# Kernel optimization log

Hardware: AMD Instinct MI355X
Metric: run time of the kernel (lower is better)

The kernel has to match this reference:

```python
import jax, jax.numpy as jnp
import numpy as np

B, H, T, K, V = 4, 16, 2048, 128, 128


def setup_inputs() -> dict:
    key = jax.random.key(0)
    ks = jax.random.split(key, 5)
    q = jax.random.normal(ks[0], (B, H, T, K), dtype=jnp.float32)
    k = jax.random.normal(ks[1], (B, H, T, K), dtype=jnp.float32)
    v = jax.random.normal(ks[2], (B, H, T, V), dtype=jnp.float32)
    # g is a per-step log decay gate: small negative so exp(g) in (0.95, 1]
    g = -jax.random.uniform(ks[3], (B, H, T), dtype=jnp.float32) * 0.05
    # beta is the delta-rule step size, in (0, 1)
    beta = jax.random.uniform(ks[4], (B, H, T), dtype=jnp.float32)
    initial_state = jnp.zeros((B, H, K, V), dtype=jnp.float32)
    return {"q": q, "k": k, "v": v, "g": g, "beta": beta,
            "initial_state": initial_state}


def _l2norm(x, eps=1e-12):
    # matches F.normalize(p=2, dim=-1): x / max(||x||_2, eps)
    n = jnp.sqrt(jnp.sum(x * x, axis=-1, keepdims=True))
    return x / jnp.maximum(n, eps)


def reference(q, k, v, g, beta, initial_state):
    q = _l2norm(q)
    k = _l2norm(k)
    scale = q.shape[-1] ** -0.5  # default scale of chunk_gated_delta_rule

    # time-major for scan: [T, B, H, ...]
    qT = jnp.moveaxis(q, 2, 0) * scale
    kT = jnp.moveaxis(k, 2, 0)
    vT = jnp.moveaxis(v, 2, 0)
    gT = jnp.moveaxis(g, 2, 0)
    bT = jnp.moveaxis(beta, 2, 0)

    def step(S, inp):
        qt, kt, vt, gt, bt = inp  # qt/kt: [B,H,K], vt: [B,H,V], gt/bt: [B,H]
        S = S * jnp.exp(gt)[..., None, None]           # gated decay of state
        kS = jnp.einsum('bhk,bhkv->bhv', kt, S)        # current prediction
        dv = bt[..., None] * (vt - kS)                 # delta-rule correction
        S = S + jnp.einsum('bhk,bhv->bhkv', kt, dv)    # rank-1 state update
        ot = jnp.einsum('bhk,bhkv->bhv', qt, S)        # readout
        return S, ot

    final_state, oT = jax.lax.scan(step, initial_state, (qT, kT, vT, gT, bT))
    o = jnp.moveaxis(oT, 0, 2)  # [B,H,T,V]
    return o, final_state
```

## Files before the change

### kernel.cpp

```cpp
#include <hip/hip_runtime.h>
#include <math.h>

typedef float f32x16 __attribute__((ext_vector_type(16)));
typedef short s16x8 __attribute__((ext_vector_type(8)));
typedef unsigned int u32;

namespace {
constexpr int B_ = 4, H_ = 16, T_ = 2048, K_ = 128, V_ = 128;
constexpr int BHn = B_ * H_;
constexpr int C = 32;
constexpr int NCH = T_ / C;
constexpr int NS = 4;
constexpr int VS = V_ / NS;
constexpr float SCALE = 0.08838834764831845f;
constexpr int SK = 136;
constexpr int SRT = 36;
constexpr int SF = 36;
constexpr size_t WSCH = 4608;
}

__device__ __forceinline__ ushort f2bf(float x) {
  unsigned u = __builtin_bit_cast(unsigned, x);
  u += 0x7FFF + ((u >> 16) & 1);
  return (ushort)(u >> 16);
}
__device__ __forceinline__ u32 cvtpk(float lo, float hi) {
  u32 r;
  asm("v_cvt_pk_bf16_f32 %0, %1, %2" : "=v"(r) : "v"(lo), "v"(hi));
  return r;
}
__device__ __forceinline__ int rowmap(int i, int lh) { return (i & 3) + 8 * (i >> 2) + 4 * lh; }

__device__ __forceinline__ void bar_lds() {
  asm volatile("s_waitcnt lgkmcnt(0)" ::: "memory");
  __builtin_amdgcn_s_barrier();
  asm volatile("" ::: "memory");
}

__device__ __forceinline__ s16x8 ld8u(const ushort* p) {
  uint2 a = *(const uint2*)(p);
  uint2 b = *(const uint2*)(p + 4);
  int4 r = make_int4((int)a.x, (int)a.y, (int)b.x, (int)b.y);
  return __builtin_bit_cast(s16x8, r);
}

__device__ __forceinline__ void packq(const f32x16& a, u32* u) {
  #pragma unroll
  for (int j = 0; j < 4; ++j) {
    u[2*j]   = cvtpk(a[4*j],   a[4*j+1]);
    u[2*j+1] = cvtpk(a[4*j+2], a[4*j+3]);
  }
}
__device__ __forceinline__ void swapfr(const u32* u, s16x8& f0, s16x8& f1) {
  u32 a0 = u[0], b0 = u[2], a1 = u[1], b1 = u[3];
  u32 a2 = u[4], b2 = u[6], a3 = u[5], b3 = u[7];
  asm("v_permlane32_swap_b32 %0, %1" : "+v"(a0), "+v"(b0));
  asm("v_permlane32_swap_b32 %0, %1" : "+v"(a1), "+v"(b1));
  asm("v_permlane32_swap_b32 %0, %1" : "+v"(a2), "+v"(b2));
  asm("v_permlane32_swap_b32 %0, %1" : "+v"(a3), "+v"(b3));
  f0 = __builtin_bit_cast(s16x8, make_int4((int)a0, (int)a1, (int)b0, (int)b1));
  f1 = __builtin_bit_cast(s16x8, make_int4((int)a2, (int)a3, (int)b2, (int)b3));
}

#define MFMA __builtin_amdgcn_mfma_f32_32x32x16_bf16

__device__ __forceinline__ f32x16 mm8(const ushort* A, const ushort* B, int lr, int lh) {
  f32x16 a0, a1;
  #pragma unroll
  for (int i = 0; i < 16; ++i) { a0[i] = 0.f; a1[i] = 0.f; }
  #pragma unroll
  for (int kb = 0; kb < 8; kb += 2) {
    const int o0 = lr * SK + 16 * kb + 8 * lh, o1 = o0 + 16;
    a0 = MFMA(*(const s16x8*)(A + o0), *(const s16x8*)(B + o0), a0, 0, 0, 0);
    a1 = MFMA(*(const s16x8*)(A + o1), *(const s16x8*)(B + o1), a1, 0, 0, 0);
  }
  return a0 + a1;
}

__global__ __launch_bounds__(256, 2)
void gdn_pre_kernel(const float* __restrict__ qg, const float* __restrict__ kg,
                    const float* __restrict__ gg, const float* __restrict__ bg,
                    char* __restrict__ ws)
{
  const int bid = blockIdx.x;
  const int bh = bid >> 6, ch = bid & 63;
  const int t = threadIdx.x, w = t >> 6, l = t & 63, lr = l & 31, lh = l >> 5;
  const int r8 = t >> 3, c8 = t & 7;
  const int t0 = ch * C;

  __shared__ __align__(16) ushort Kh[C * SK], Qh[C * SK];
  __shared__ __align__(16) float Mm[C * SF];
  __shared__ __align__(16) ushort Tt[C * 32], Gt[C * 32];
  __shared__ float ls_g[C], ls_b[C], ls_eb[C], ls_emb[C], ls_nq[C];

  {
    const float4* q4 = (const float4*)(qg + ((size_t)bh * T_ + t0 + r8) * K_);
    const float4* k4 = (const float4*)(kg + ((size_t)bh * T_ + t0 + r8) * K_);
    float4 qv[4], kv[4]; float sq = 0.f, sk = 0.f;
    #pragma unroll
    for (int c = 0; c < 4; ++c) {
      qv[c] = q4[c8 + 8 * c]; kv[c] = k4[c8 + 8 * c];
      sq += qv[c].x*qv[c].x + qv[c].y*qv[c].y + qv[c].z*qv[c].z + qv[c].w*qv[c].w;
      sk += kv[c].x*kv[c].x + kv[c].y*kv[c].y + kv[c].z*kv[c].z + kv[c].w*kv[c].w;
    }
    sq += __shfl_xor(sq, 1); sq += __shfl_xor(sq, 2); sq += __shfl_xor(sq, 4);
    sk += __shfl_xor(sk, 1); sk += __shfl_xor(sk, 2); sk += __shfl_xor(sk, 4);
    const float niq = SCALE / fmaxf(sqrtf(sq), 1e-12f);
    const float nik = 1.0f / fmaxf(sqrtf(sk), 1e-12f);
    if (c8 == 0) ls_nq[r8] = niq;
    #pragma unroll
    for (int c = 0; c < 4; ++c) {
      const int f4 = c8 + 8 * c;
      uint2 upk, upq;
      upk.x = cvtpk(kv[c].x * nik, kv[c].y * nik);
      upk.y = cvtpk(kv[c].z * nik, kv[c].w * nik);
      upq.x = cvtpk(qv[c].x * niq, qv[c].y * niq);
      upq.y = cvtpk(qv[c].z * niq, qv[c].w * niq);
      *(uint2*)(Kh + r8 * SK + f4 * 4) = upk;
      *(uint2*)(Qh + r8 * SK + f4 * 4) = upq;
    }
    if (t < C)          ls_g[t]     = gg[(size_t)bh * T_ + t0 + t];
    else if (t < 2 * C) ls_b[t - C] = bg[(size_t)bh * T_ + t0 + t - C];
  }
  __syncthreads();
  if (w == 3 && l < 32) {
    float x = ls_g[l];
    #pragma unroll
    for (int d = 1; d < 32; d <<= 1) { float y = __shfl_up(x, d); if (l >= d) x += y; }
    ls_eb[l] = expf(x); ls_emb[l] = expf(-x);
  }
  if (w == 0) {
    f32x16 acc = mm8(Kh, Kh, lr, lh);
    #pragma unroll
    for (int i = 0; i < 16; ++i) Mm[rowmap(i, lh) * SF + lr] = acc[i];
  }
  if (w == 1) {
    f32x16 acc = mm8(Qh, Kh, lr, lh);
    #pragma unroll
    for (int i = 0; i < 16; ++i) {
      int row = rowmap(i, lh);
      Gt[row * 32 + lr] = (lr <= row) ? f2bf(acc[i]) : (ushort)0;
    }
  }
  __syncthreads();
  if (w == 2 && l < 32) {
    const int j = l;
    float x[32];
    #pragma unroll
    for (int m = 0; m < 32; ++m) x[m] = (m == j) ? 1.f : 0.f;
    #pragma unroll
    for (int r = 1; r < 32; ++r) {
      const float* mr = Mm + r * SF;
      float p0 = 0.f, p1 = 0.f, p2 = 0.f, p3 = 0.f;
      #pragma unroll
      for (int jb = 0; jb + 4 <= r; jb += 4) {
        float4 m4 = *(const float4*)(mr + jb);
        p0 = fmaf(m4.x, x[jb + 0], p0);
        p1 = fmaf(m4.y, x[jb + 1], p1);
        p2 = fmaf(m4.z, x[jb + 2], p2);
        p3 = fmaf(m4.w, x[jb + 3], p3);
      }
      #pragma unroll
      for (int m = (r & ~3); m < r; ++m) p1 = fmaf(mr[m], x[m], p1);
      float xr = -ls_b[r] * ((p0 + p1) + (p2 + p3));
      if (r > j) x[r] = xr;
    }
    #pragma unroll
    for (int r = 0; r < 32; ++r) Tt[r * 32 + j] = f2bf(x[r]);
  }
  __syncthreads();
  {
    char* wsb = ws + ((size_t)bh * NCH + ch) * WSCH;
    u32* wT = (u32*)wsb; u32* wG = (u32*)(wsb + 2048); float* wS = (float*)(wsb + 4096);
    const u32* sT = (const u32*)Tt; const u32* sG = (const u32*)Gt;
    wT[t] = sT[t]; wT[t + 256] = sT[t + 256];
    wG[t] = sG[t]; wG[t + 256] = sG[t + 256];
    if (t < 32)      wS[t] = ls_eb[t];
    else if (t < 96) {
      int j = t - 32, r = j >> 1;
      wS[t] = (j & 1) ? ls_b[r] : ls_b[r] * ls_emb[r];
    } else if (t < 128) wS[t] = ls_nq[t - 96];
  }
}

__global__ __launch_bounds__(256, 1)
void gdn_seq_kernel(const float* __restrict__ qg, const float* __restrict__ kg,
                    const float* __restrict__ vg, const float* __restrict__ s0,
                    const char* __restrict__ ws, float* __restrict__ out)
{
  const int bid = blockIdx.x;
  const int xcd = bid & 7, qd = bid >> 3;
  const int bh = (qd >> 2) * 8 + xcd;
  const int v0 = (qd & 3) * VS;
  const int t = threadIdx.x, w = t >> 6, l = t & 63, lr = l & 31, lh = l >> 5;
  const int ts = t & 127;
  const int r4 = ts >> 2, c4 = ts & 3;

  __shared__ __align__(16) ushort Kh[2][C * SK];
  __shared__ __align__(16) ushort KhT[2][K_ * SRT];
  __shared__ __align__(16) float  ls_eb[3][C];
  __shared__ __align__(16) float  ls_bbf[2][2 * C];
  __shared__ __align__(16) ushort Sfr[2][8][64 * 8];
  __shared__ __align__(16) ushort Ufr[2][2][64 * 8];

  const float* qh = qg + (size_t)bh * T_ * K_;
  const float* kh = kg + (size_t)bh * T_ * K_;
  const float* vh = vg + (size_t)bh * T_ * V_;
  const char* wsh = ws + (size_t)bh * NCH * WSCH;
  float* oh = out + (size_t)bh * T_ * V_;

  f32x16 Sst[4];
  s16x8 Sfrag[8];
  float pvvA[16], pvvB[16];
  s16x8 pTfA[2], pTfB[2];
  if (w == 0) {
    #pragma unroll
    for (int q = 0; q < 4; ++q) {
      const float* sp = s0 + ((size_t)bh * K_ + 32 * q) * V_ + v0 + lr;
      #pragma unroll
      for (int i = 0; i < 16; i += 2) {
        int row = rowmap(i, lh);
        Sst[q][i]     = sp[(size_t)row * V_];
        Sst[q][i + 1] = sp[(size_t)(row + 1) * V_];
      }
      u32 us[8]; packq(Sst[q], us);
      swapfr(us, Sfrag[2 * q], Sfrag[2 * q + 1]);
      *(s16x8*)(&Sfr[0][2 * q][l * 8])     = Sfrag[2 * q];
      *(s16x8*)(&Sfr[0][2 * q + 1][l * 8]) = Sfrag[2 * q + 1];
    }
    {
      const float* vb = vh + (size_t)v0 + lr;
      #pragma unroll
      for (int i = 0; i < 16; ++i) pvvA[i] = vb[(size_t)rowmap(i, lh) * V_];
      const ushort* Tg = (const ushort*)wsh;
      pTfA[0] = *(const s16x8*)(Tg + lr * 32 + 8 * lh);
      pTfA[1] = *(const s16x8*)(Tg + lr * 32 + 16 + 8 * lh);
    }
  }

  float4 pq4[16]; float pniq = 0.f;
  s16x8 pGf[2];
  f32x16 Xprev;
  auto qprefetch = [&](int cc) {
    const float4* q4 = (const float4*)(qh + (size_t)(cc * C + lr) * K_);
    #pragma unroll
    for (int kb = 0; kb < 8; ++kb) {
      pq4[2 * kb]     = q4[4 * kb + 2 * lh];
      pq4[2 * kb + 1] = q4[4 * kb + 2 * lh + 1];
    }
    pniq = ((const float*)(wsh + (size_t)cc * WSCH + 4096))[96 + lr];
  };

  float4 pk[8]; float psc = 0.f;
  auto prefetch = [&](int cc) {
    const float4* k4 = (const float4*)(kh + (size_t)(cc * C + r4) * K_);
    #pragma unroll
    for (int j = 0; j < 8; ++j) pk[j] = k4[c4 + 4 * j];
    psc = (ts < 96) ? ((const float*)(wsh + (size_t)cc * WSCH + 4096))[ts] : 0.f;
  };
  auto stage = [&](int b, int b3) {
    float sk = 0.f;
    #pragma unroll
    for (int j = 0; j < 8; ++j)
      sk += pk[j].x*pk[j].x + pk[j].y*pk[j].y + pk[j].z*pk[j].z + pk[j].w*pk[j].w;
    sk += __shfl_xor(sk, 1); sk += __shfl_xor(sk, 2);
    const float nik = 1.0f / fmaxf(sqrtf(sk), 1e-12f);
    #pragma unroll
    for (int j = 0; j < 8; ++j) {
      const int f4 = c4 + 4 * j;
      uint2 upk;
      upk.x = cvtpk(pk[j].x * nik, pk[j].y * nik);
      upk.y = cvtpk(pk[j].z * nik, pk[j].w * nik);
      *(uint2*)(&Kh[b][0] + r4 * SK + 4 * f4) = upk;
      ushort* kt = &KhT[b][0] + (4 * f4) * SRT + r4;
      kt[0]       = (ushort)upk.x;
      kt[SRT]     = (ushort)(upk.x >> 16);
      kt[2 * SRT] = (ushort)upk.y;
      kt[3 * SRT] = (ushort)(upk.y >> 16);
    }
    if (ts < 32)      ls_eb[b3][ts]      = psc;
    else if (ts < 96) ls_bbf[b][ts - 32] = psc;
  };

  if (w >= 2)      { prefetch(0); stage(0, 0); prefetch(1); }
  else if (w == 1) { qprefetch(0); }
  bar_lds();

  auto iter = [&](int ch, int cur, float* pvvC, float* pvvN, s16x8* pTfC, s16x8* pTfN) {
    const int nxt = cur ^ 1, c3 = ch % 3;
    if (w == 0) {
      if (ch + 1 < NCH) {
        const float* vb = vh + (size_t)((ch + 1) * C) * V_ + v0 + lr;
        #pragma unroll
        for (int i = 0; i < 16; ++i) pvvN[i] = vb[(size_t)rowmap(i, lh) * V_];
        const ushort* Tg = (const ushort*)(wsh + (size_t)(ch + 1) * WSCH);
        pTfN[0] = *(const s16x8*)(Tg + lr * 32 + 8 * lh);
        pTfN[1] = *(const s16x8*)(Tg + lr * 32 + 16 + 8 * lh);
      }
      s16x8 kt2[8];
      #pragma unroll
      for (int q = 0; q < 4; ++q) {
        kt2[2*q]   = ld8u(&KhT[cur][0] + (32 * q + lr) * SRT + 8 * lh);
        kt2[2*q+1] = ld8u(&KhT[cur][0] + (32 * q + lr) * SRT + 16 + 8 * lh);
      }
      float2 bbp[16];
      #pragma unroll
      for (int p = 0; p < 8; ++p) {
        int row = rowmap(2 * p, lh);
        bbp[2*p]   = ((const float2*)ls_bbf[cur])[row];
        bbp[2*p+1] = ((const float2*)ls_bbf[cur])[row + 1];
      }
      float tv[16];
      #pragma unroll
      for (int i = 0; i < 16; ++i) tv[i] = bbp[i].x * pvvC[i];
      f32x16 wa0, wa1, wa2, wa3;
      #pragma unroll
      for (int i = 0; i < 16; ++i) { wa0[i]=0.f; wa1[i]=0.f; wa2[i]=0.f; wa3[i]=0.f; }
      const ushort* khc = &Kh[cur][0] + lr * SK + 8 * lh;
      wa0 = MFMA(*(const s16x8*)(khc +   0), Sfrag[0], wa0, 0, 0, 0);
      wa1 = MFMA(*(const s16x8*)(khc +  16), Sfrag[1], wa1, 0, 0, 0);
      wa2 = MFMA(*(const s16x8*)(khc +  32), Sfrag[2], wa2, 0, 0, 0);
      wa3 = MFMA(*(const s16x8*)(khc +  48), Sfrag[3], wa3, 0, 0, 0);
      wa0 = MFMA(*(const s16x8*)(khc +  64), Sfrag[4], wa0, 0, 0, 0);
      wa1 = MFMA(*(const s16x8*)(khc +  80), Sfrag[5], wa1, 0, 0, 0);
      wa2 = MFMA(*(const s16x8*)(khc +  96), Sfrag[6], wa2, 0, 0, 0);
      wa3 = MFMA(*(const s16x8*)(khc + 112), Sfrag[7], wa3, 0, 0, 0);
      f32x16 Wacc = (wa0 + wa1) + (wa2 + wa3);
      f32x16 Bv;
      #pragma unroll
      for (int i = 0; i < 16; ++i) Bv[i] = tv[i] - bbp[i].y * Wacc[i];
      u32 ub[8]; packq(Bv, ub);
      s16x8 bf0, bf1; swapfr(ub, bf0, bf1);
      f32x16 Uacc;
      #pragma unroll
      for (int i = 0; i < 16; ++i) Uacc[i] = 0.f;
      Uacc = MFMA(pTfC[0], bf0, Uacc, 0, 0, 0);
      Uacc = MFMA(pTfC[1], bf1, Uacc, 0, 0, 0);
      u32 uu[8]; packq(Uacc, uu);
      s16x8 uf0, uf1; swapfr(uu, uf0, uf1);
      *(s16x8*)(&Ufr[cur][0][l * 8]) = uf0;
      *(s16x8*)(&Ufr[cur][1][l * 8]) = uf1;
      const float ebL = ls_eb[c3][31];
      #pragma unroll
      for (int q = 0; q < 4; ++q) {
        f32x16 acc = Sst[q];
        acc = MFMA(kt2[2*q],   uf0, acc, 0, 0, 0);
        acc = MFMA(kt2[2*q+1], uf1, acc, 0, 0, 0);
        #pragma unroll
        for (int i = 0; i < 16; ++i) Sst[q][i] = ebL * acc[i];
        u32 us[8]; packq(Sst[q], us);
        swapfr(us, Sfrag[2 * q], Sfrag[2 * q + 1]);
        *(s16x8*)(&Sfr[nxt][2 * q][l * 8])     = Sfrag[2 * q];
        *(s16x8*)(&Sfr[nxt][2 * q + 1][l * 8]) = Sfrag[2 * q + 1];
      }
    } else if (w == 1) {
      f32x16 x0, x1, x2, x3;
      #pragma unroll
      for (int i = 0; i < 16; ++i) { x0[i]=0.f; x1[i]=0.f; x2[i]=0.f; x3[i]=0.f; }
      #pragma unroll
      for (int kb = 0; kb < 8; ++kb) {
        u32 ca = cvtpk(pq4[2*kb].x * pniq,   pq4[2*kb].y * pniq);
        u32 cb = cvtpk(pq4[2*kb].z * pniq,   pq4[2*kb].w * pniq);
        u32 cc2 = cvtpk(pq4[2*kb+1].x * pniq, pq4[2*kb+1].y * pniq);
        u32 cd = cvtpk(pq4[2*kb+1].z * pniq, pq4[2*kb+1].w * pniq);
        s16x8 qa = __builtin_bit_cast(s16x8, make_int4((int)ca,(int)cb,(int)cc2,(int)cd));
        s16x8 sb = *(const s16x8*)(&Sfr[cur][kb][l * 8]);
        switch (kb & 3) {
          case 0: x0 = MFMA(qa, sb, x0, 0, 0, 0); break;
          case 1: x1 = MFMA(qa, sb, x1, 0, 0, 0); break;
          case 2: x2 = MFMA(qa, sb, x2, 0, 0, 0); break;
          default: x3 = MFMA(qa, sb, x3, 0, 0, 0); break;
        }
      }
      f32x16 Xn = (x0 + x1) + (x2 + x3);
      if (ch > 0) {
        const int pc = nxt, p3 = (ch - 1) % 3, tp = (ch - 1) * C;
        f32x16 Oacc = Xprev;
        Oacc = MFMA(pGf[0], *(const s16x8*)(&Ufr[pc][0][l * 8]), Oacc, 0, 0, 0);
        Oacc = MFMA(pGf[1], *(const s16x8*)(&Ufr[pc][1][l * 8]), Oacc, 0, 0, 0);
        #pragma unroll
        for (int i = 0; i < 16; ++i) {
          const int row = rowmap(i, lh);
          oh[(size_t)(tp + row) * V_ + v0 + lr] = ls_eb[p3][row] * Oacc[i];
        }
      }
      Xprev = Xn;
      {
        const ushort* Gg = (const ushort*)(wsh + (size_t)ch * WSCH + 2048);
        pGf[0] = *(const s16x8*)(Gg + lr * 32 + 8 * lh);
        pGf[1] = *(const s16x8*)(Gg + lr * 32 + 16 + 8 * lh);
      }
      if (ch + 1 < NCH) qprefetch(ch + 1);
    } else {
      if (ch + 1 < NCH) stage(nxt, (ch + 1) % 3);
      if (ch + 2 < NCH) prefetch(ch + 2);
    }
    bar_lds();
  };

  for (int ch = 0; ch < NCH; ch += 2) {
    iter(ch,     0, pvvA, pvvB, pTfA, pTfB);
    iter(ch + 1, 1, pvvB, pvvA, pTfB, pTfA);
  }

  if (w == 1) {
    const int pc = (NCH - 1) & 1, p3 = (NCH - 1) % 3, tp = (NCH - 1) * C;
    f32x16 Oacc = Xprev;
    Oacc = MFMA(pGf[0], *(const s16x8*)(&Ufr[pc][0][l * 8]), Oacc, 0, 0, 0);
    Oacc = MFMA(pGf[1], *(const s16x8*)(&Ufr[pc][1][l * 8]), Oacc, 0, 0, 0);
    #pragma unroll
    for (int i = 0; i < 16; ++i) {
      const int row = rowmap(i, lh);
      oh[(size_t)(tp + row) * V_ + v0 + lr] = ls_eb[p3][row] * Oacc[i];
    }
  }
  if (w == 0) {
    #pragma unroll
    for (int q = 0; q < 4; ++q) {
      float* sp = out + (size_t)BHn * T_ * V_
                      + ((size_t)bh * K_ + 32 * q) * V_ + v0 + lr;
      #pragma unroll
      for (int i = 0; i < 16; ++i)
        sp[(size_t)rowmap(i, lh) * V_] = Sst[q][i];
    }
  }
}
#undef MFMA

extern "C" void kernel_launch(void* const* d_in, const int* in_sizes, int n_in,
                              void* d_out, int out_size, void* d_ws, size_t ws_size,
                              hipStream_t stream) {
  const float* q    = (const float*)d_in[0];
  const float* k    = (const float*)d_in[1];
  const float* v    = (const float*)d_in[2];
  const float* g    = (const float*)d_in[3];
  const float* beta = (const float*)d_in[4];
  const float* s0   = (const float*)d_in[5];
  float* out = (float*)d_out;
  char* ws = (char*)d_ws;
  hipLaunchKernelGGL(gdn_pre_kernel, dim3(BHn * NCH), dim3(256), 0, stream,
                     q, k, g, beta, ws);
  hipLaunchKernelGGL(gdn_seq_kernel, dim3(BHn * NS), dim3(256), 0, stream,
                     q, k, v, s0, ws, out);
}
```

Measured before the change: 155.8 us.

## Fold decay scaling into precompute and restructure per-chunk prefetch schedule

The per-row decay factor is folded into the precomputed G matrix and the q-norm scalars. The sequential kernel no longer keeps a three-deep decay buffer or rescales each output element; it reads only the last-row decay value. The K-chunk prefetch is now double-buffered so the next load is issued before staging. V and T prefetches move to after their last use, so single register buffers replace the A/B pairs, and the output epilogue for the previous chunk runs before the new q·S MFMAs. The aim is to cut register pressure and shorten the per-chunk critical path, at the cost of extra registers for the second K buffer and a changed workspace layout.

```diff
diff --git a/kernel.cpp b/kernel.cpp
--- a/kernel.cpp
+++ b/kernel.cpp
@@ -134,15 +134,16 @@
     #pragma unroll
     for (int i = 0; i < 16; ++i) Mm[rowmap(i, lh) * SF + lr] = acc[i];
   }
+  f32x16 gacc;
+  if (w == 1) gacc = mm8(Qh, Kh, lr, lh);
+  __syncthreads();
   if (w == 1) {
-    f32x16 acc = mm8(Qh, Kh, lr, lh);
     #pragma unroll
     for (int i = 0; i < 16; ++i) {
       int row = rowmap(i, lh);
-      Gt[row * 32 + lr] = (lr <= row) ? f2bf(acc[i]) : (ushort)0;
-    }
-  }
-  __syncthreads();
+      Gt[row * 32 + lr] = (lr <= row) ? f2bf(ls_eb[row] * gacc[i]) : (ushort)0;
+    }
+  }
   if (w == 2 && l < 32) {
     const int j = l;
     float x[32];
@@ -175,11 +176,11 @@
     const u32* sT = (const u32*)Tt; const u32* sG = (const u32*)Gt;
     wT[t] = sT[t]; wT[t + 256] = sT[t + 256];
     wG[t] = sG[t]; wG[t + 256] = sG[t + 256];
-    if (t < 32)      wS[t] = ls_eb[t];
-    else if (t < 96) {
-      int j = t - 32, r = j >> 1;
-      wS[t] = (j & 1) ? ls_b[r] : ls_b[r] * ls_emb[r];
-    } else if (t < 128) wS[t] = ls_nq[t - 96];
+    if (t < 64) {
+      int r = t >> 1;
+      wS[t] = (t & 1) ? ls_b[r] : ls_b[r] * ls_emb[r];
+    } else if (t < 96) wS[t] = ls_nq[t - 64] * ls_eb[t - 64];
+    else if (t == 96)  wS[96] = ls_eb[31];
   }
 }
 
@@ -198,8 +199,8 @@
 
   __shared__ __align__(16) ushort Kh[2][C * SK];
   __shared__ __align__(16) ushort KhT[2][K_ * SRT];
-  __shared__ __align__(16) float  ls_eb[3][C];
   __shared__ __align__(16) float  ls_bbf[2][2 * C];
+  __shared__ float  ls_ebL[2];
   __shared__ __align__(16) ushort Sfr[2][8][64 * 8];
   __shared__ __align__(16) ushort Ufr[2][2][64 * 8];
 
@@ -211,8 +212,8 @@
 
   f32x16 Sst[4];
   s16x8 Sfrag[8];
-  float pvvA[16], pvvB[16];
-  s16x8 pTfA[2], pTfB[2];
+  float pvv[16];
+  s16x8 pTf[2];
   if (w == 0) {
     #pragma unroll
     for (int q = 0; q < 4; ++q) {
@@ -231,10 +232,10 @@
     {
       const float* vb = vh + (size_t)v0 + lr;
       #pragma unroll
-      for (int i = 0; i < 16; ++i) pvvA[i] = vb[(size_t)rowmap(i, lh) * V_];
+      for (int i = 0; i < 16; ++i) pvv[i] = vb[(size_t)rowmap(i, lh) * V_];
       const ushort* Tg = (const ushort*)wsh;
-      pTfA[0] = *(const s16x8*)(Tg + lr * 32 + 8 * lh);
-      pTfA[1] = *(const s16x8*)(Tg + lr * 32 + 16 + 8 * lh);
+      pTf[0] = *(const s16x8*)(Tg + lr * 32 + 8 * lh);
+      pTf[1] = *(const s16x8*)(Tg + lr * 32 + 16 + 8 * lh);
     }
   }
 
@@ -248,17 +249,18 @@
       pq4[2 * kb]     = q4[4 * kb + 2 * lh];
       pq4[2 * kb + 1] = q4[4 * kb + 2 * lh + 1];
     }
-    pniq = ((const float*)(wsh + (size_t)cc * WSCH + 4096))[96 + lr];
+    pniq = ((const float*)(wsh + (size_t)cc * WSCH + 4096))[64 + lr];
   };
 
-  float4 pk[8]; float psc = 0.f;
-  auto prefetch = [&](int cc) {
+  float4 pkA[8], pkB[8]; float pscA = 0.f, pscB = 0.f;
+  auto prefetch = [&](int cc, float4* pkd, float& pscd) {
     const float4* k4 = (const float4*)(kh + (size_t)(cc * C + r4) * K_);
     #pragma unroll
-    for (int j = 0; j < 8; ++j) pk[j] = k4[c4 + 4 * j];
-    psc = (ts < 96) ? ((const float*)(wsh + (size_t)cc * WSCH + 4096))[ts] : 0.f;
+    for (int j = 0; j < 8; ++j) pkd[j] = k4[c4 + 4 * j];
+    const float* scal = (const float*)(wsh + (size_t)cc * WSCH + 4096);
+    pscd = (ts < 64) ? scal[ts] : (ts == 64 ? scal[96] : 0.f);
   };
-  auto stage = [&](int b, int b3) {
+  auto stage = [&](int b, const float4* pk, float psc) {
     float sk = 0.f;
     #pragma unroll
     for (int j = 0; j < 8; ++j)
@@ -278,31 +280,18 @@
       kt[2 * SRT] = (ushort)upk.y;
       kt[3 * SRT] = (ushort)(upk.y >> 16);
     }
-    if (ts < 32)      ls_eb[b3][ts]      = psc;
-    else if (ts < 96) ls_bbf[b][ts - 32] = psc;
+    if (ts < 64)       ls_bbf[b][ts] = psc;
+    else if (ts == 64) ls_ebL[b]     = psc;
   };
 
-  if (w >= 2)      { prefetch(0); stage(0, 0); prefetch(1); }
-  else if (w == 1) { qprefetch(0); }
+  if (w >= 2) {
+    prefetch(0, pkA, pscA); stage(0, pkA, pscA); prefetch(1, pkA, pscA);
+  } else if (w == 1) { qprefetch(0); }
   bar_lds();
 
-  auto iter = [&](int ch, int cur, float* pvvC, float* pvvN, s16x8* pTfC, s16x8* pTfN) {
-    const int nxt = cur ^ 1, c3 = ch % 3;
+  auto iter = [&](int ch, int cur, float4* pkC, float4* pkN, float& pscC, float& pscN) {
+    const int nxt = cur ^ 1;
     if (w == 0) {
-      if (ch + 1 < NCH) {
-        const float* vb = vh + (size_t)((ch + 1) * C) * V_ + v0 + lr;
-        #pragma unroll
-        for (int i = 0; i < 16; ++i) pvvN[i] = vb[(size_t)rowmap(i, lh) * V_];
-        const ushort* Tg = (const ushort*)(wsh + (size_t)(ch + 1) * WSCH);
-        pTfN[0] = *(const s16x8*)(Tg + lr * 32 + 8 * lh);
-        pTfN[1] = *(const s16x8*)(Tg + lr * 32 + 16 + 8 * lh);
-      }
-      s16x8 kt2[8];
-      #pragma unroll
-      for (int q = 0; q < 4; ++q) {
-        kt2[2*q]   = ld8u(&KhT[cur][0] + (32 * q + lr) * SRT + 8 * lh);
-        kt2[2*q+1] = ld8u(&KhT[cur][0] + (32 * q + lr) * SRT + 16 + 8 * lh);
-      }
       float2 bbp[16];
       #pragma unroll
       for (int p = 0; p < 8; ++p) {
@@ -312,7 +301,18 @@
       }
       float tv[16];
       #pragma unroll
-      for (int i = 0; i < 16; ++i) tv[i] = bbp[i].x * pvvC[i];
+      for (int i = 0; i < 16; ++i) tv[i] = bbp[i].x * pvv[i];
+      if (ch + 1 < NCH) {
+        const float* vb = vh + (size_t)((ch + 1) * C) * V_ + v0 + lr;
+        #pragma unroll
+        for (int i = 0; i < 16; ++i) pvv[i] = vb[(size_t)rowmap(i, lh) * V_];
+      }
+      s16x8 kt2[8];
+      #pragma unroll
+      for (int q = 0; q < 4; ++q) {
+        kt2[2*q]   = ld8u(&KhT[cur][0] + (32 * q + lr) * SRT + 8 * lh);
+        kt2[2*q+1] = ld8u(&KhT[cur][0] + (32 * q + lr) * SRT + 16 + 8 * lh);
+      }
       f32x16 wa0, wa1, wa2, wa3;
       #pragma unroll
       for (int i = 0; i < 16; ++i) { wa0[i]=0.f; wa1[i]=0.f; wa2[i]=0.f; wa3[i]=0.f; }
@@ -334,13 +334,18 @@
       f32x16 Uacc;
       #pragma unroll
       for (int i = 0; i < 16; ++i) Uacc[i] = 0.f;
-      Uacc = MFMA(pTfC[0], bf0, Uacc, 0, 0, 0);
-      Uacc = MFMA(pTfC[1], bf1, Uacc, 0, 0, 0);
+      Uacc = MFMA(pTf[0], bf0, Uacc, 0, 0, 0);
+      Uacc = MFMA(pTf[1], bf1, Uacc, 0, 0, 0);
+      if (ch + 1 < NCH) {
+        const ushort* Tg = (const ushort*)(wsh + (size_t)(ch + 1) * WSCH);
+        pTf[0] = *(const s16x8*)(Tg + lr * 32 + 8 * lh);
+        pTf[1] = *(const s16x8*)(Tg + lr * 32 + 16 + 8 * lh);
+      }
       u32 uu[8]; packq(Uacc, uu);
       s16x8 uf0, uf1; swapfr(uu, uf0, uf1);
       *(s16x8*)(&Ufr[cur][0][l * 8]) = uf0;
       *(s16x8*)(&Ufr[cur][1][l * 8]) = uf1;
-      const float ebL = ls_eb[c3][31];
+      const float ebL = ls_ebL[cur];
       #pragma unroll
       for (int q = 0; q < 4; ++q) {
         f32x16 acc = Sst[q];
@@ -354,9 +359,25 @@
         *(s16x8*)(&Sfr[nxt][2 * q + 1][l * 8]) = Sfrag[2 * q + 1];
       }
     } else if (w == 1) {
-      f32x16 x0, x1, x2, x3;
-      #pragma unroll
-      for (int i = 0; i < 16; ++i) { x0[i]=0.f; x1[i]=0.f; x2[i]=0.f; x3[i]=0.f; }
+      if (ch > 0) {
+        const int pc = nxt, tp = (ch - 1) * C;
+        f32x16 Oacc = Xprev;
+        Oacc = MFMA(pGf[0], *(const s16x8*)(&Ufr[pc][0][l * 8]), Oacc, 0, 0, 0);
+        Oacc = MFMA(pGf[1], *(const s16x8*)(&Ufr[pc][1][l * 8]), Oacc, 0, 0, 0);
+        #pragma unroll
+        for (int i = 0; i < 16; ++i) {
+          const int row = rowmap(i, lh);
+          oh[(size_t)(tp + row) * V_ + v0 + lr] = Oacc[i];
+        }
+      }
+      {
+        const ushort* Gg = (const ushort*)(wsh + (size_t)ch * WSCH + 2048);
+        pGf[0] = *(const s16x8*)(Gg + lr * 32 + 8 * lh);
+        pGf[1] = *(const s16x8*)(Gg + lr * 32 + 16 + 8 * lh);
+      }
+      f32x16 x0, x1;
+      #pragma unroll
+      for (int i = 0; i < 16; ++i) { x0[i]=0.f; x1[i]=0.f; }
       #pragma unroll
       for (int kb = 0; kb < 8; ++kb) {
         u32 ca = cvtpk(pq4[2*kb].x * pniq,   pq4[2*kb].y * pniq);
@@ -365,53 +386,32 @@
         u32 cd = cvtpk(pq4[2*kb+1].z * pniq, pq4[2*kb+1].w * pniq);
         s16x8 qa = __builtin_bit_cast(s16x8, make_int4((int)ca,(int)cb,(int)cc2,(int)cd));
         s16x8 sb = *(const s16x8*)(&Sfr[cur][kb][l * 8]);
-        switch (kb & 3) {
-          case 0: x0 = MFMA(qa, sb, x0, 0, 0, 0); break;
-          case 1: x1 = MFMA(qa, sb, x1, 0, 0, 0); break;
-          case 2: x2 = MFMA(qa, sb, x2, 0, 0, 0); break;
-          default: x3 = MFMA(qa, sb, x3, 0, 0, 0); break;
-        }
-      }
-      f32x16 Xn = (x0 + x1) + (x2 + x3);
-      if (ch > 0) {
-        const int pc = nxt, p3 = (ch - 1) % 3, tp = (ch - 1) * C;
-        f32x16 Oacc = Xprev;
-        Oacc = MFMA(pGf[0], *(const s16x8*)(&Ufr[pc][0][l * 8]), Oacc, 0, 0, 0);
-        Oacc = MFMA(pGf[1], *(const s16x8*)(&Ufr[pc][1][l * 8]), Oacc, 0, 0, 0);
-        #pragma unroll
-        for (int i = 0; i < 16; ++i) {
-          const int row = rowmap(i, lh);
-          oh[(size_t)(tp + row) * V_ + v0 + lr] = ls_eb[p3][row] * Oacc[i];
-        }
-      }
-      Xprev = Xn;
-      {
-        const ushort* Gg = (const ushort*)(wsh + (size_t)ch * WSCH + 2048);
-        pGf[0] = *(const s16x8*)(Gg + lr * 32 + 8 * lh);
-        pGf[1] = *(const s16x8*)(Gg + lr * 32 + 16 + 8 * lh);
-      }
+        if (kb & 1) x1 = MFMA(qa, sb, x1, 0, 0, 0);
+        else        x0 = MFMA(qa, sb, x0, 0, 0, 0);
+      }
+      Xprev = x0 + x1;
       if (ch + 1 < NCH) qprefetch(ch + 1);
     } else {
-      if (ch + 1 < NCH) stage(nxt, (ch + 1) % 3);
-      if (ch + 2 < NCH) prefetch(ch + 2);
+      if (ch + 2 < NCH) prefetch(ch + 2, pkN, pscN);
+      if (ch + 1 < NCH) stage(nxt, pkC, pscC);
     }
     bar_lds();
   };
 
   for (int ch = 0; ch < NCH; ch += 2) {
-    iter(ch,     0, pvvA, pvvB, pTfA, pTfB);
-    iter(ch + 1, 1, pvvB, pvvA, pTfB, pTfA);
+    iter(ch,     0, pkA, pkB, pscA, pscB);
+    iter(ch + 1, 1, pkB, pkA, pscB, pscA);
   }
 
   if (w == 1) {
-    const int pc = (NCH - 1) & 1, p3 = (NCH - 1) % 3, tp = (NCH - 1) * C;
+    const int pc = (NCH - 1) & 1, tp = (NCH - 1) * C;
     f32x16 Oacc = Xprev;
     Oacc = MFMA(pGf[0], *(const s16x8*)(&Ufr[pc][0][l * 8]), Oacc, 0, 0, 0);
     Oacc = MFMA(pGf[1], *(const s16x8*)(&Ufr[pc][1][l * 8]), Oacc, 0, 0, 0);
     #pragma unroll
     for (int i = 0; i < 16; ++i) {
       const int row = rowmap(i, lh);
-      oh[(size_t)(tp + row) * V_ + v0 + lr] = ls_eb[p3][row] * Oacc[i];
+      oh[(size_t)(tp + row) * V_ + v0 + lr] = Oacc[i];
     }
   }
   if (w == 0) {
```

Measured after the change: 157.1 us. No clear change (+0.8%).
